# Kernel optimization log

Hardware: AMD Instinct MI355X
Metric: run time of the kernel (lower is better)

The kernel has to match this reference:

```python
import jax, jax.numpy as jnp
import numpy as np

B, N, D = 1, 512, 128


def setup_inputs() -> dict:
    key = jax.random.key(0)
    ks = jax.random.split(key, 8)
    h = jax.random.normal(ks[0], (B, N, D), dtype=jnp.float32)
    rel_emb = jax.random.normal(ks[1], (B, N, N, D), dtype=jnp.float32)
    edge_mask = jax.random.bernoulli(ks[2], 0.5, (B, N, N))
    s2d = 1.0 / np.sqrt(2 * D)
    s1d = 1.0 / np.sqrt(D)
    return {
        "h": h,
        "rel_emb": rel_emb,
        "edge_mask": edge_mask,
        "msg_w1": jax.random.normal(ks[3], (2 * D, D), dtype=jnp.float32) * s2d,
        "msg_b1": jnp.zeros((D,), jnp.float32),
        "msg_w2": jax.random.normal(ks[4], (D, D), dtype=jnp.float32) * s1d,
        "msg_b2": jnp.zeros((D,), jnp.float32),
        "upd_w1": jax.random.normal(ks[5], (2 * D, D), dtype=jnp.float32) * s2d,
        "upd_b1": jnp.zeros((D,), jnp.float32),
        "upd_w2": jax.random.normal(ks[6], (D, D), dtype=jnp.float32) * s1d,
        "upd_b2": jnp.zeros((D,), jnp.float32),
        "ln_g": jnp.ones((D,), jnp.float32),
        "ln_b": jnp.zeros((D,), jnp.float32),
    }


def _layernorm(x, g, b, eps=1e-5):
    mu = x.mean(-1, keepdims=True)
    var = x.var(-1, keepdims=True)
    return (x - mu) * jax.lax.rsqrt(var + eps) * g + b


def reference(h, rel_emb, edge_mask, msg_w1, msg_b1, msg_w2, msg_b2,
              upd_w1, upd_b1, upd_w2, upd_b2, ln_g, ln_b):
    _, n, d = h.shape
    # msg_in = cat([h_j, e_ji]); h_j[b,i,j] = h[b,j], e_ji[b,i,j] = rel_emb[b,j,i]
    # Split first linear so the h-dependent part is computed once per sender j.
    w1_h, w1_e = msg_w1[:d], msg_w1[d:]
    hj_part = h @ w1_h                                   # [B,N,D], indexed by sender j
    e_ji = jnp.swapaxes(rel_emb, 1, 2)                   # [B,N(i),N(j),D]
    pre = hj_part[:, None, :, :] + jnp.einsum('bijd,de->bije', e_ji, w1_e) + msg_b1
    msgs = jax.nn.silu(pre) @ msg_w2 + msg_b2            # [B,N,N,D]
    mask = jnp.swapaxes(edge_mask, 1, 2).astype(h.dtype)  # [B,N(i),N(j)]
    agg = jnp.einsum('bijd,bij->bid', msgs, mask)        # masked sum over senders j
    upd_in = jnp.concatenate([h, agg], axis=-1)          # [B,N,2D]
    delta = jax.nn.silu(upd_in @ upd_w1 + upd_b1) @ upd_w2 + upd_b2
    return _layernorm(h + delta, ln_g, ln_b)
```

## Files before the change

### kernel.cpp

```cpp
#include <hip/hip_runtime.h>
#include <hip/hip_bf16.h>

#define NN 512
#define DD 128

typedef __bf16 bf16x8 __attribute__((ext_vector_type(8)));
typedef float f32x4 __attribute__((ext_vector_type(4)));

static __device__ __forceinline__ f32x4 mfma16(bf16x8 a, bf16x8 b, f32x4 c) {
  return __builtin_amdgcn_mfma_f32_16x16x32_bf16(a, b, c, 0, 0, 0);
}

__global__ void k_pre(const float* __restrict__ h,
                      const float* __restrict__ msg_w1,
                      const float* __restrict__ msg_b1,
                      const int* __restrict__ emask,
                      __bf16* __restrict__ w1t, float* __restrict__ hjp,
                      float* __restrict__ cnt) {
  __shared__ float hr[128];
  __shared__ int csum;
  int j = blockIdx.x, t = threadIdx.x;
  if (t == 0) csum = 0;
  hr[t] = h[j * 128 + t];
  __syncthreads();
  float acc = msg_b1[t];
  #pragma unroll 16
  for (int k = 0; k < 128; k++) acc += hr[k] * msg_w1[k * 128 + t];
  hjp[j * 128 + t] = acc;
  if (t < 32) {
    int tt = j * 32 + t;
    int e = tt >> 7, k = tt & 127;
    w1t[e * 128 + k] = (__bf16)msg_w1[(128 + k) * 128 + e];
  }
  int s = 0;
  #pragma unroll
  for (int r = 0; r < 4; r++) s += emask[(t * 4 + r) * NN + j] ? 1 : 0;
  #pragma unroll
  for (int off = 32; off > 0; off >>= 1) s += __shfl_down(s, off, 64);
  if ((t & 63) == 0) atomicAdd(&csum, s);
  __syncthreads();
  if (t == 0) cnt[j] = (float)csum;
}

#define CVT(bf, xa, xb) { \
  bf[0] = (__bf16)xa[0]; bf[1] = (__bf16)xa[1]; \
  bf[2] = (__bf16)xa[2]; bf[3] = (__bf16)xa[3]; \
  bf[4] = (__bf16)xb[0]; bf[5] = (__bf16)xb[1]; \
  bf[6] = (__bf16)xb[2]; bf[7] = (__bf16)xb[3]; }

__global__ __launch_bounds__(256, 2) void k_main(
    const float* __restrict__ rel, const int* __restrict__ emask,
    const float* __restrict__ hjp, const __bf16* __restrict__ w1t_g,
    float* __restrict__ partial) {
  __shared__ __align__(16) __bf16 tile[2 * 16 * 136];
  __shared__ float mk[256];
  const int tid = threadIdx.x;
  const int wave = tid >> 6;
  const int lane = tid & 63;
  const int l15 = lane & 15;
  const int q = lane >> 4;

  const int it = blockIdx.x >> 5;
  const int jc = blockIdx.x & 31;
  const int irow = it * 16;
  const int jbase = jc * 16;

  mk[tid] = emask[(size_t)(jbase + (tid >> 4)) * NN + irow + (tid & 15)] ? 1.f : 0.f;

  bf16x8 aw00, aw01, aw02, aw03, aw10, aw11, aw12, aw13;
  {
    const __bf16* b0 = w1t_g + (wave * 32 + l15) * 128 + q * 8;
    aw00 = *(const bf16x8*)(b0);
    aw01 = *(const bf16x8*)(b0 + 32);
    aw02 = *(const bf16x8*)(b0 + 64);
    aw03 = *(const bf16x8*)(b0 + 96);
    const __bf16* b1 = b0 + 16 * 128;
    aw10 = *(const bf16x8*)(b1);
    aw11 = *(const bf16x8*)(b1 + 32);
    aw12 = *(const bf16x8*)(b1 + 64);
    aw13 = *(const bf16x8*)(b1 + 96);
  }

  f32x4 t0 = {0.f, 0.f, 0.f, 0.f}, t1 = t0;

  const int srow = tid >> 4;
  const int schunk = tid & 15;
  const float* sb = rel + ((size_t)jbase * NN + irow + srow) * DD + schunk * 8;
  __bf16* sd = tile + srow * 136 + schunk * 8;

  __syncthreads();

  f32x4 xa0 = {0.f, 0.f, 0.f, 0.f}, xb0 = xa0;
  f32x4 xa1 = xa0, xb1 = xa0;
  {
    if (mk[srow] != 0.f) { xa0 = *(const f32x4*)sb; xb0 = *(const f32x4*)(sb + 4); }
    bf16x8 pub;
    CVT(pub, xa0, xb0)
    *(bf16x8*)sd = pub;
    xa0 = {0.f, 0.f, 0.f, 0.f}; xb0 = xa0;
    if (mk[16 + srow] != 0.f) {
      const float* s = sb + (size_t)NN * DD;
      xa0 = *(const f32x4*)s; xb0 = *(const f32x4*)(s + 4);
    }
    if (mk[32 + srow] != 0.f) {
      const float* s = sb + 2 * (size_t)NN * DD;
      xa1 = *(const f32x4*)s; xb1 = *(const f32x4*)(s + 4);
    }
  }

  #define COMPUTE(JROW, BUFOFF) { \
    const float ms = mk[(JROW) * 16 + l15]; \
    const __bf16* tp = tile + (BUFOFF) + l15 * 136 + q * 8; \
    bf16x8 bf0 = *(const bf16x8*)(tp); \
    bf16x8 bf1 = *(const bf16x8*)(tp + 32); \
    bf16x8 bf2 = *(const bf16x8*)(tp + 64); \
    bf16x8 bf3 = *(const bf16x8*)(tp + 96); \
    f32x4 p0 = {0.f, 0.f, 0.f, 0.f}, p1 = p0; \
    p0 = mfma16(aw00, bf0, p0); p1 = mfma16(aw10, bf0, p1); \
    p0 = mfma16(aw01, bf1, p0); p1 = mfma16(aw11, bf1, p1); \
    p0 = mfma16(aw02, bf2, p0); p1 = mfma16(aw12, bf2, p1); \
    p0 = mfma16(aw03, bf3, p0); p1 = mfma16(aw13, bf3, p1); \
    const float* hj = hjp + (size_t)(jbase + (JROW)) * DD + wave * 32 + q * 4; \
    f32x4 hv0 = *(const f32x4*)(hj); \
    f32x4 hv1 = *(const f32x4*)(hj + 16); \
    _Pragma("unroll") \
    for (int r = 0; r < 4; r++) { \
      float v0 = p0[r] + hv0[r]; \
      float v1 = p1[r] + hv1[r]; \
      t0[r] += ms * v0 * __builtin_amdgcn_rcpf(1.f + __expf(-v0)); \
      t1[r] += ms * v1 * __builtin_amdgcn_rcpf(1.f + __expf(-v1)); \
    } }

  #pragma unroll 1
  for (int jj = 0; jj < 16; jj += 2) {
    __syncthreads();
    {
      bf16x8 pub;
      CVT(pub, xa0, xb0)
      *(bf16x8*)(sd + 2176) = pub;
      if (jj + 3 < 16) {
        if (mk[(jj + 3) * 16 + srow] != 0.f) {
          const float* s = sb + (size_t)(jj + 3) * NN * DD;
          xa0 = *(const f32x4*)s; xb0 = *(const f32x4*)(s + 4);
        }
      }
    }
    COMPUTE(jj, 0)

    __syncthreads();
    {
      if (jj + 2 < 16) {
        bf16x8 pub;
        CVT(pub, xa1, xb1)
        *(bf16x8*)sd = pub;
      }
      if (jj + 4 < 16) {
        if (mk[(jj + 4) * 16 + srow] != 0.f) {
          const float* s = sb + (size_t)(jj + 4) * NN * DD;
          xa1 = *(const f32x4*)s; xb1 = *(const f32x4*)(s + 4);
        }
      }
    }
    COMPUTE(jj + 1, 2176)
  }
  #undef COMPUTE

  float* pp = partial + ((size_t)jc * NN + irow + l15) * DD + wave * 32 + q * 4;
  *(f32x4*)pp = t0;
  *(f32x4*)(pp + 16) = t1;
}

__global__ void k_update(const float* __restrict__ h, const float* __restrict__ partial,
                         const float* __restrict__ w2, const float* __restrict__ b2,
                         const float* __restrict__ cnt,
                         const float* __restrict__ uw1, const float* __restrict__ ub1,
                         const float* __restrict__ uw2, const float* __restrict__ ub2,
                         const float* __restrict__ g, const float* __restrict__ bb,
                         float* __restrict__ out) {
  __shared__ float Trow[128];
  __shared__ float uin[256];
  __shared__ float zl[128];
  __shared__ float ss[4];
  int i = blockIdx.x, t = threadIdx.x;
  float hv = h[i * 128 + t];
  float ts = 0.f;
  #pragma unroll
  for (int c = 0; c < 32; c++) ts += partial[((size_t)c * NN + i) * DD + t];
  Trow[t] = ts;
  __syncthreads();
  float a = cnt[i] * b2[t];
  #pragma unroll 16
  for (int e = 0; e < 128; e++) a += Trow[e] * w2[e * 128 + t];
  uin[t] = hv;
  uin[128 + t] = a;
  __syncthreads();
  float z = ub1[t];
  #pragma unroll 16
  for (int k = 0; k < 256; k++) z += uin[k] * uw1[k * 128 + t];
  z = z / (1.f + __expf(-z));
  zl[t] = z;
  __syncthreads();
  float dl = ub2[t];
  #pragma unroll 16
  for (int k = 0; k < 128; k++) dl += zl[k] * uw2[k * 128 + t];
  float x = hv + dl;
  float s1 = x, s2 = x * x;
  #pragma unroll
  for (int off = 32; off > 0; off >>= 1) {
    s1 += __shfl_down(s1, off, 64);
    s2 += __shfl_down(s2, off, 64);
  }
  if ((t & 63) == 0) { ss[(t >> 6) * 2] = s1; ss[(t >> 6) * 2 + 1] = s2; }
  __syncthreads();
  s1 = ss[0] + ss[2];
  s2 = ss[1] + ss[3];
  float mu = s1 * (1.f / 128.f);
  float var = s2 * (1.f / 128.f) - mu * mu;
  out[i * 128 + t] = (x - mu) * rsqrtf(var + 1e-5f) * g[t] + bb[t];
}

extern "C" void kernel_launch(void* const* d_in, const int* in_sizes, int n_in,
                              void* d_out, int out_size, void* d_ws, size_t ws_size,
                              hipStream_t stream) {
  const float* h      = (const float*)d_in[0];
  const float* rel    = (const float*)d_in[1];
  const int*   emask  = (const int*)d_in[2];
  const float* msg_w1 = (const float*)d_in[3];
  const float* msg_b1 = (const float*)d_in[4];
  const float* msg_w2 = (const float*)d_in[5];
  const float* msg_b2 = (const float*)d_in[6];
  const float* upd_w1 = (const float*)d_in[7];
  const float* upd_b1 = (const float*)d_in[8];
  const float* upd_w2 = (const float*)d_in[9];
  const float* upd_b2 = (const float*)d_in[10];
  const float* ln_g   = (const float*)d_in[11];
  const float* ln_b   = (const float*)d_in[12];
  float* out = (float*)d_out;

  char* ws = (char*)d_ws;
  float*  hjp     = (float*)ws;
  __bf16* w1t     = (__bf16*)(ws + 262144);
  float*  cnt     = (float*)(ws + 262144 + 32768);
  float*  partial = (float*)(ws + 262144 + 36864);

  k_pre<<<512, 128, 0, stream>>>(h, msg_w1, msg_b1, emask, w1t, hjp, cnt);
  k_main<<<1024, 256, 0, stream>>>(rel, emask, hjp, w1t, partial);
  k_update<<<512, 128, 0, stream>>>(h, partial, msg_w2, msg_b2, cnt,
                                    upd_w1, upd_b1, upd_w2, upd_b2,
                                    ln_g, ln_b, out);
}
```

Measured before the change: 46.31 us.

## Deepen rel_emb prefetch to four stages, stage hjp in LDS, split accumulators

The main kernel now keeps four register prefetch buffers in flight instead of two, issuing global loads of rel_emb five rows ahead so more memory latency overlaps compute. The per-sender hjp rows are copied once into shared memory instead of being re-read from global memory in every compute step. The small matvec loops in the pre and update kernels use multiple independent accumulators to break the serial FMA dependency chains. The cost is more registers per thread, which may pressure the occupancy target of 2 blocks per SM, plus 8KB of extra LDS per block.

```diff
diff --git a/kernel.cpp b/kernel.cpp
--- a/kernel.cpp
+++ b/kernel.cpp
@@ -23,10 +23,13 @@
   if (t == 0) csum = 0;
   hr[t] = h[j * 128 + t];
   __syncthreads();
-  float acc = msg_b1[t];
-  #pragma unroll 16
-  for (int k = 0; k < 128; k++) acc += hr[k] * msg_w1[k * 128 + t];
-  hjp[j * 128 + t] = acc;
+  float a0 = msg_b1[t], a1 = 0.f;
+  #pragma unroll 16
+  for (int k = 0; k < 128; k += 2) {
+    a0 += hr[k] * msg_w1[k * 128 + t];
+    a1 += hr[k + 1] * msg_w1[(k + 1) * 128 + t];
+  }
+  hjp[j * 128 + t] = a0 + a1;
   if (t < 32) {
     int tt = j * 32 + t;
     int e = tt >> 7, k = tt & 127;
@@ -54,6 +57,7 @@
     float* __restrict__ partial) {
   __shared__ __align__(16) __bf16 tile[2 * 16 * 136];
   __shared__ float mk[256];
+  __shared__ __align__(16) float hjl[16 * 128];
   const int tid = threadIdx.x;
   const int wave = tid >> 6;
   const int lane = tid & 63;
@@ -66,6 +70,12 @@
   const int jbase = jc * 16;
 
   mk[tid] = emask[(size_t)(jbase + (tid >> 4)) * NN + irow + (tid & 15)] ? 1.f : 0.f;
+  {
+    int r2 = tid >> 4, c8 = (tid & 15) * 8;
+    const float* hsrc = hjp + (size_t)(jbase + r2) * DD + c8;
+    *(f32x4*)(hjl + r2 * 128 + c8) = *(const f32x4*)hsrc;
+    *(f32x4*)(hjl + r2 * 128 + c8 + 4) = *(const f32x4*)(hsrc + 4);
+  }
 
   bf16x8 aw00, aw01, aw02, aw03, aw10, aw11, aw12, aw13;
   {
@@ -92,12 +102,14 @@
 
   f32x4 xa0 = {0.f, 0.f, 0.f, 0.f}, xb0 = xa0;
   f32x4 xa1 = xa0, xb1 = xa0;
+  f32x4 xa2 = xa0, xb2 = xa0;
+  f32x4 xa3 = xa0, xb3 = xa0;
   {
-    if (mk[srow] != 0.f) { xa0 = *(const f32x4*)sb; xb0 = *(const f32x4*)(sb + 4); }
+    f32x4 ra = xa0, rb = xa0;
+    if (mk[srow] != 0.f) { ra = *(const f32x4*)sb; rb = *(const f32x4*)(sb + 4); }
     bf16x8 pub;
-    CVT(pub, xa0, xb0)
+    CVT(pub, ra, rb)
     *(bf16x8*)sd = pub;
-    xa0 = {0.f, 0.f, 0.f, 0.f}; xb0 = xa0;
     if (mk[16 + srow] != 0.f) {
       const float* s = sb + (size_t)NN * DD;
       xa0 = *(const f32x4*)s; xb0 = *(const f32x4*)(s + 4);
@@ -106,11 +118,19 @@
       const float* s = sb + 2 * (size_t)NN * DD;
       xa1 = *(const f32x4*)s; xb1 = *(const f32x4*)(s + 4);
     }
-  }
-
-  #define COMPUTE(JROW, BUFOFF) { \
+    if (mk[48 + srow] != 0.f) {
+      const float* s = sb + 3 * (size_t)NN * DD;
+      xa2 = *(const f32x4*)s; xb2 = *(const f32x4*)(s + 4);
+    }
+    if (mk[64 + srow] != 0.f) {
+      const float* s = sb + 4 * (size_t)NN * DD;
+      xa3 = *(const f32x4*)s; xb3 = *(const f32x4*)(s + 4);
+    }
+  }
+
+  #define COMPUTE(JROW) { \
     const float ms = mk[(JROW) * 16 + l15]; \
-    const __bf16* tp = tile + (BUFOFF) + l15 * 136 + q * 8; \
+    const __bf16* tp = tile + (((JROW) & 1) ? 2176 : 0) + l15 * 136 + q * 8; \
     bf16x8 bf0 = *(const bf16x8*)(tp); \
     bf16x8 bf1 = *(const bf16x8*)(tp + 32); \
     bf16x8 bf2 = *(const bf16x8*)(tp + 64); \
@@ -120,7 +140,7 @@
     p0 = mfma16(aw01, bf1, p0); p1 = mfma16(aw11, bf1, p1); \
     p0 = mfma16(aw02, bf2, p0); p1 = mfma16(aw12, bf2, p1); \
     p0 = mfma16(aw03, bf3, p0); p1 = mfma16(aw13, bf3, p1); \
-    const float* hj = hjp + (size_t)(jbase + (JROW)) * DD + wave * 32 + q * 4; \
+    const float* hj = hjl + (JROW) * 128 + wave * 32 + q * 4; \
     f32x4 hv0 = *(const f32x4*)(hj); \
     f32x4 hv1 = *(const f32x4*)(hj + 16); \
     _Pragma("unroll") \
@@ -131,38 +151,29 @@
       t1[r] += ms * v1 * __builtin_amdgcn_rcpf(1.f + __expf(-v1)); \
     } }
 
+  #define STEP(JR, XA, XB) { \
+    __syncthreads(); \
+    if ((JR) + 1 < 16) { \
+      bf16x8 pub; \
+      CVT(pub, XA, XB) \
+      *(bf16x8*)(sd + ((((JR) + 1) & 1) ? 2176 : 0)) = pub; \
+    } \
+    if ((JR) + 5 < 16) { \
+      if (mk[((JR) + 5) * 16 + srow] != 0.f) { \
+        const float* s = sb + (size_t)((JR) + 5) * NN * DD; \
+        XA = *(const f32x4*)s; XB = *(const f32x4*)(s + 4); \
+      } \
+    } \
+    COMPUTE(JR) }
+
   #pragma unroll 1
-  for (int jj = 0; jj < 16; jj += 2) {
-    __syncthreads();
-    {
-      bf16x8 pub;
-      CVT(pub, xa0, xb0)
-      *(bf16x8*)(sd + 2176) = pub;
-      if (jj + 3 < 16) {
-        if (mk[(jj + 3) * 16 + srow] != 0.f) {
-          const float* s = sb + (size_t)(jj + 3) * NN * DD;
-          xa0 = *(const f32x4*)s; xb0 = *(const f32x4*)(s + 4);
-        }
-      }
-    }
-    COMPUTE(jj, 0)
-
-    __syncthreads();
-    {
-      if (jj + 2 < 16) {
-        bf16x8 pub;
-        CVT(pub, xa1, xb1)
-        *(bf16x8*)sd = pub;
-      }
-      if (jj + 4 < 16) {
-        if (mk[(jj + 4) * 16 + srow] != 0.f) {
-          const float* s = sb + (size_t)(jj + 4) * NN * DD;
-          xa1 = *(const f32x4*)s; xb1 = *(const f32x4*)(s + 4);
-        }
-      }
-    }
-    COMPUTE(jj + 1, 2176)
-  }
+  for (int jj = 0; jj < 16; jj += 4) {
+    STEP(jj,     xa0, xb0)
+    STEP(jj + 1, xa1, xb1)
+    STEP(jj + 2, xa2, xb2)
+    STEP(jj + 3, xa3, xb3)
+  }
+  #undef STEP
   #undef COMPUTE
 
   float* pp = partial + ((size_t)jc * NN + irow + l15) * DD + wave * 32 + q * 4;
@@ -188,22 +199,34 @@
   for (int c = 0; c < 32; c++) ts += partial[((size_t)c * NN + i) * DD + t];
   Trow[t] = ts;
   __syncthreads();
-  float a = cnt[i] * b2[t];
-  #pragma unroll 16
-  for (int e = 0; e < 128; e++) a += Trow[e] * w2[e * 128 + t];
+  float a0 = cnt[i] * b2[t], a1 = 0.f;
+  #pragma unroll 16
+  for (int e = 0; e < 128; e += 2) {
+    a0 += Trow[e] * w2[e * 128 + t];
+    a1 += Trow[e + 1] * w2[(e + 1) * 128 + t];
+  }
   uin[t] = hv;
-  uin[128 + t] = a;
-  __syncthreads();
-  float z = ub1[t];
-  #pragma unroll 16
-  for (int k = 0; k < 256; k++) z += uin[k] * uw1[k * 128 + t];
+  uin[128 + t] = a0 + a1;
+  __syncthreads();
+  float z0 = ub1[t], z1 = 0.f, z2 = 0.f, z3 = 0.f;
+  #pragma unroll 16
+  for (int k = 0; k < 256; k += 4) {
+    z0 += uin[k] * uw1[k * 128 + t];
+    z1 += uin[k + 1] * uw1[(k + 1) * 128 + t];
+    z2 += uin[k + 2] * uw1[(k + 2) * 128 + t];
+    z3 += uin[k + 3] * uw1[(k + 3) * 128 + t];
+  }
+  float z = (z0 + z1) + (z2 + z3);
   z = z / (1.f + __expf(-z));
   zl[t] = z;
   __syncthreads();
-  float dl = ub2[t];
-  #pragma unroll 16
-  for (int k = 0; k < 128; k++) dl += zl[k] * uw2[k * 128 + t];
-  float x = hv + dl;
+  float d0 = ub2[t], d1 = 0.f;
+  #pragma unroll 16
+  for (int k = 0; k < 128; k += 2) {
+    d0 += zl[k] * uw2[k * 128 + t];
+    d1 += zl[k + 1] * uw2[(k + 1) * 128 + t];
+  }
+  float x = hv + d0 + d1;
   float s1 = x, s2 = x * x;
   #pragma unroll
   for (int off = 32; off > 0; off >>= 1) {
```

Result: faster. 43.16 us, median of 2 (-6.8%).
